# Kernel optimization log

Measured on AMD Instinct MI355X. Metric: run time of the kernel, lower is better.

The kernel has to match this reference:

```python
import jax, jax.numpy as jnp
import numpy as np

N_NODES = 50000
N_EDGES = 800000
NFEAT = 128
NHID = 128
NCLASS = 10
NUM_GRAPHS = 512


def setup_inputs() -> dict:
    key = jax.random.key(0)
    ks = jax.random.split(key, 12)
    x = jax.random.normal(ks[0], (N_NODES, NFEAT), dtype=jnp.float32)
    edge_index = jax.random.randint(ks[1], (2, N_EDGES), 0, N_NODES, dtype=jnp.int64)
    batch = jnp.sort(jax.random.randint(ks[2], (N_NODES,), 0, NUM_GRAPHS, dtype=jnp.int64))
    def glorot(k, fan_in, fan_out):
        lim = np.sqrt(6.0 / (fan_in + fan_out))
        return jax.random.uniform(k, (fan_in, fan_out), jnp.float32, -lim, lim)
    return {
        "x": x, "edge_index": edge_index, "batch": batch,
        "W0": glorot(ks[3], NFEAT, NHID), "b0": jnp.zeros((NHID,), jnp.float32),
        "W1": glorot(ks[4], NHID, NHID), "b1": jnp.zeros((NHID,), jnp.float32),
        "W2": glorot(ks[5], NHID, NHID), "b2": jnp.zeros((NHID,), jnp.float32),
        "lin_w": glorot(ks[6], NHID, NCLASS), "lin_b": jnp.zeros((NCLASS,), jnp.float32),
    }


def _gcn_norm(edge_index, n):
    # PyG GCNConv: add self-loops, symmetric normalization D^-1/2 A D^-1/2
    loop = jnp.arange(n, dtype=edge_index.dtype)
    src = jnp.concatenate([edge_index[0], loop])  # [E+N]
    dst = jnp.concatenate([edge_index[1], loop])
    deg = jax.ops.segment_sum(jnp.ones_like(dst, dtype=jnp.float32), dst, num_segments=n)
    dis = jnp.where(deg > 0, jax.lax.rsqrt(jnp.maximum(deg, 1.0)), 0.0)
    norm = dis[src] * dis[dst]  # [E+N]
    return src, dst, norm


def _gcn_conv(x, W, b, src, dst, norm, n):
    h = x @ W                              # [N, nhid]
    msg = h[src] * norm[:, None]           # gather + scale, [E+N, nhid]
    out = jax.ops.segment_sum(msg, dst, num_segments=n)
    return out + b


def reference(x, edge_index, batch, W0, b0, W1, b1, W2, b2, lin_w, lin_b):
    n = x.shape[0]
    src, dst, norm = _gcn_norm(edge_index, n)
    h = x
    for (W, b) in ((W0, b0), (W1, b1), (W2, b2)):
        h = jax.nn.relu(_gcn_conv(h, W, b, src, dst, norm, n))
    # global mean pool over graphs
    sums = jax.ops.segment_sum(h, batch, num_segments=NUM_GRAPHS)
    cnts = jax.ops.segment_sum(jnp.ones((n,), jnp.float32), batch, num_segments=NUM_GRAPHS)
    pooled = sums / jnp.maximum(cnts, 1.0)[:, None]  # [G, nhid]
    logits = pooled @ lin_w + lin_b
    return jax.nn.log_softmax(logits, axis=-1)
```

## Files before the change

kernel.cpp:

```cpp
#include <hip/hip_runtime.h>
#include <hip/hip_fp16.h>


#define FEAT 128
#define NCLASS 10
#define NB_MAX 512

typedef _Float16 h8 __attribute__((ext_vector_type(8)));
typedef float f4 __attribute__((ext_vector_type(4)));

__device__ inline int swz(int row, int cbyte) { return row * 256 + (cbyte ^ ((row & 7) << 4)); }

__device__ inline void gather_pad8(const h8* __restrict__ Hs, const int* __restrict__ csr,
                                   int s, int e, int lig, float* a0, float* a1) {
  int ep = s + ((e - s + 7) & ~7);
  for (int k = s; k < ep; k += 8) {
    int4 c0 = *(const int4*)&csr[k];
    int4 c1 = *(const int4*)&csr[k + 4];
    h8 v0 = Hs[(size_t)c0.x * 16 + lig];
    h8 v1 = Hs[(size_t)c0.y * 16 + lig];
    h8 v2 = Hs[(size_t)c0.z * 16 + lig];
    h8 v3 = Hs[(size_t)c0.w * 16 + lig];
    h8 v4 = Hs[(size_t)c1.x * 16 + lig];
    h8 v5 = Hs[(size_t)c1.y * 16 + lig];
    h8 v6 = Hs[(size_t)c1.z * 16 + lig];
    h8 v7 = Hs[(size_t)c1.w * 16 + lig];
#pragma unroll
    for (int j = 0; j < 8; ++j) a0[j] += (float)v0[j];
#pragma unroll
    for (int j = 0; j < 8; ++j) a1[j] += (float)v1[j];
#pragma unroll
    for (int j = 0; j < 8; ++j) a0[j] += (float)v2[j];
#pragma unroll
    for (int j = 0; j < 8; ++j) a1[j] += (float)v3[j];
#pragma unroll
    for (int j = 0; j < 8; ++j) a0[j] += (float)v4[j];
#pragma unroll
    for (int j = 0; j < 8; ++j) a1[j] += (float)v5[j];
#pragma unroll
    for (int j = 0; j < 8; ++j) a0[j] += (float)v6[j];
#pragma unroll
    for (int j = 0; j < 8; ++j) a1[j] += (float)v7[j];
  }
}

__global__ void __launch_bounds__(256) prep_kernel(const int* __restrict__ ei,
                                                   int* __restrict__ bhist,
                                                   int ne, int nb, int epb, int hb,
                                                   const float* __restrict__ W0,
                                                   const float* __restrict__ W1,
                                                   const float* __restrict__ W2,
                                                   _Float16* __restrict__ Wt, int wtb,
                                                   const int* __restrict__ batch,
                                                   int* __restrict__ gstart, int n, int g) {
  int t = threadIdx.x;
  if (blockIdx.x >= hb + wtb) {
    int i = (blockIdx.x - hb - wtb) * 256 + t;
    if (i >= n) return;
    int bi = batch[i];
    int bp = (i == 0) ? -1 : batch[i - 1];
    for (int q = bp + 1; q <= bi; ++q) gstart[q] = i;
    if (i == n - 1)
      for (int q = bi + 1; q <= g; ++q) gstart[q] = n;
    return;
  }
  if (blockIdx.x >= hb) {
    int i = (blockIdx.x - hb) * 256 + t;
    if (i < 3 * FEAT * FEAT) {
      int l = i / (FEAT * FEAT);
      int r = i - l * (FEAT * FEAT);
      int nn = r >> 7, kk = r & 127;
      const float* W = (l == 0) ? W0 : (l == 1) ? W1 : W2;
      Wt[i] = (_Float16)W[kk * FEAT + nn];
    }
    return;
  }
  __shared__ int lh[NB_MAX];
  for (int i = t; i < nb; i += 256) lh[i] = 0;
  __syncthreads();
  int r0 = blockIdx.x * epb;
  int r1 = min(r0 + epb, ne);
  for (int k = r0 + t; k < r1; k += 256) atomicAdd(&lh[ei[ne + k] >> 7], 1);
  __syncthreads();
  for (int i = t; i < nb; i += 256)
    if (lh[i]) atomicAdd(&bhist[i], lh[i]);
}

__global__ void __launch_bounds__(512) bscan_kernel(const int* __restrict__ bhist,
                                                    int* __restrict__ bstart,
                                                    int* __restrict__ bcur,
                                                    int nb, int ne) {
  __shared__ int sh[512];
  int t = threadIdx.x;
  int v = (t < nb) ? bhist[t] : 0;
  sh[t] = v;
  __syncthreads();
  int x = v;
  for (int d = 1; d < 512; d <<= 1) {
    int y = (t >= d) ? sh[t - d] : 0;
    __syncthreads();
    x += y;
    sh[t] = x;
    __syncthreads();
  }
  if (t < nb) {
    bstart[t] = x - v;
    bcur[t] = x - v;
  }
  if (t == 0) bstart[nb] = ne;
}

__global__ void __launch_bounds__(256) scatter_kernel(const int* __restrict__ ei,
                                                      int* __restrict__ bcur,
                                                      unsigned* __restrict__ buf,
                                                      int ne, int nb, int epb) {
  __shared__ int lh[NB_MAX], lbs[NB_MAX];
  int t = threadIdx.x;
  for (int i = t; i < nb; i += 256) lh[i] = 0;
  __syncthreads();
  int r0 = blockIdx.x * epb;
  int r1 = min(r0 + epb, ne);
  for (int k = r0 + t; k < r1; k += 256) atomicAdd(&lh[ei[ne + k] >> 7], 1);
  __syncthreads();
  for (int i = t; i < nb; i += 256) {
    int c = lh[i];
    lbs[i] = c ? atomicAdd(&bcur[i], c) : 0;
    lh[i] = 0;
  }
  __syncthreads();
  for (int k = r0 + t; k < r1; k += 256) {
    int src = ei[k];
    int dst = ei[ne + k];
    int b = dst >> 7;
    int p = lbs[b] + atomicAdd(&lh[b], 1);
    buf[p] = (unsigned)src | ((unsigned)(dst & 127) << 25);
  }
}

__global__ void __launch_bounds__(256) bucket_build_kernel(const unsigned* __restrict__ buf,
                                                           const int* __restrict__ bstart,
                                                           int2* __restrict__ offend,
                                                           int* __restrict__ csr,
                                                           float* __restrict__ dis, int n) {
  __shared__ int cnt[128], cur[128], sh[128], ps[128];
  int b = blockIdx.x, t = threadIdx.x;
  int e0 = bstart[b], e1 = bstart[b + 1];
  int pb = ((e0 + 7) & ~7) + 1024 * b;
  if (t < 128) cnt[t] = 0;
  __syncthreads();
  for (int k = e0 + t; k < e1; k += 256) atomicAdd(&cnt[buf[k] >> 25], 1);
  __syncthreads();
  int v = 0, pdv = 0;
  if (t < 128) {
    v = cnt[t];
    pdv = (v + 7) & ~7;
    sh[t] = pdv;
  }
  __syncthreads();
  int x = pdv;
  for (int d = 1; d < 128; d <<= 1) {
    int y = (t < 128 && t >= d) ? sh[t - d] : 0;
    __syncthreads();
    if (t < 128) {
      x += y;
      sh[t] = x;
    }
    __syncthreads();
  }
  if (t < 128) {
    int node = (b << 7) + t;
    int st = x - pdv;
    ps[t] = st;
    cur[t] = st;
    if (node < n) {
      offend[node] = make_int2(pb + st, pb + st + v);
      dis[node] = rsqrtf((float)(v + 1));
    }
  }
  __syncthreads();
  for (int k = e0 + t; k < e1; k += 256) {
    unsigned u = buf[k];
    int d = u >> 25;
    int p = atomicAdd(&cur[d], 1);
    csr[pb + p] = (int)(u & 0x1FFFFFFu);
  }
  __syncthreads();
  if (t < 128) {
    int pd = (cnt[t] + 7) & ~7;
    for (int q = cnt[t]; q < pd; ++q) csr[pb + ps[t] + q] = n;
  }
}

__global__ void __launch_bounds__(256) gemm_mfma_kernel(const float* __restrict__ Xf,
                                                        const _Float16* __restrict__ Wt,
                                                        const float* __restrict__ dis,
                                                        _Float16* __restrict__ Hs, int n) {
  __shared__ _Float16 st[64 * FEAT];
  int tid = threadIdx.x;
  int w = tid >> 6, lane = tid & 63;
  int l15 = lane & 15, hi = lane >> 4;

  int rowA = blockIdx.x * 64 + w * 16 + l15;
  int rA = min(rowA, n - 1);

  f4 acc[8];
#pragma unroll
  for (int nb = 0; nb < 8; ++nb) acc[nb] = (f4)(0.f);

#pragma unroll
  for (int kk = 0; kk < FEAT; kk += 32) {
    int ko = kk + hi * 8;
    h8 a;
    float4 x0 = *(const float4*)&Xf[(size_t)rA * FEAT + ko];
    float4 x1 = *(const float4*)&Xf[(size_t)rA * FEAT + ko + 4];
    a[0] = (_Float16)x0.x; a[1] = (_Float16)x0.y; a[2] = (_Float16)x0.z; a[3] = (_Float16)x0.w;
    a[4] = (_Float16)x1.x; a[5] = (_Float16)x1.y; a[6] = (_Float16)x1.z; a[7] = (_Float16)x1.w;
#pragma unroll
    for (int nb = 0; nb < 8; ++nb) {
      h8 bfr = *(const h8*)&Wt[(nb * 16 + l15) * FEAT + ko];
      acc[nb] = __builtin_amdgcn_mfma_f32_16x16x32_f16(a, bfr, acc[nb], 0, 0, 0);
    }
  }

  float dv[4];
#pragma unroll
  for (int r = 0; r < 4; ++r) {
    int grow = blockIdx.x * 64 + w * 16 + hi * 4 + r;
    dv[r] = dis[min(grow, n - 1)];
  }
#pragma unroll
  for (int nb = 0; nb < 8; ++nb)
#pragma unroll
    for (int r = 0; r < 4; ++r)
      st[(w * 16 + hi * 4 + r) * FEAT + nb * 16 + l15] = (_Float16)(acc[nb][r] * dv[r]);
  __syncthreads();

  int rowbase = blockIdx.x * 64;
#pragma unroll
  for (int i = tid; i < 64 * FEAT / 8; i += 256) {
    int row = rowbase + (i >> 4);
    if (row < n)
      *(uint4*)&Hs[(size_t)row * FEAT + (i & 15) * 8] =
          *(const uint4*)&st[(i >> 4) * FEAT + (i & 15) * 8];
  }
}

__global__ void __launch_bounds__(256) fused_kernel(const h8* __restrict__ Hs_in,
                                                    const int* __restrict__ csr,
                                                    const int2* __restrict__ offend,
                                                    const float* __restrict__ dis,
                                                    const float* __restrict__ bias,
                                                    const _Float16* __restrict__ Wt,
                                                    _Float16* __restrict__ Hs_out, int n) {
  __shared__ char xsb[64 * 256];
  int tid = threadIdx.x;
  int w = tid >> 6, lane = tid & 63;
  int grp = lane >> 4, lig = lane & 15;
  int row0 = blockIdx.x * 64;
  int g16 = w * 4 + grp;

  float4 b0 = ((const float4*)bias)[lig * 2];
  float4 b1 = ((const float4*)bias)[lig * 2 + 1];
  float bb[8] = {b0.x, b0.y, b0.z, b0.w, b1.x, b1.y, b1.z, b1.w};

  for (int m = 0; m < 4; ++m) {
    int ar = g16 * 4 + m;
    int nd = min(row0 + ar, n - 1);
    int2 oe = offend[nd];
    float a0[8], a1[8];
    h8 v = Hs_in[(size_t)nd * 16 + lig];
#pragma unroll
    for (int j = 0; j < 8; ++j) {
      a0[j] = (float)v[j];
      a1[j] = 0.f;
    }
    gather_pad8(Hs_in, csr, oe.x, oe.y, lig, a0, a1);
    float d = dis[nd];
    h8 o;
#pragma unroll
    for (int j = 0; j < 8; ++j)
      o[j] = (_Float16)fmaxf(fmaf(d, a0[j] + a1[j], bb[j]), 0.f);
    *(h8*)(xsb + swz(ar, lig * 16)) = o;
  }
  __syncthreads();

  int l15 = lane & 15, hi = lane >> 4;
  f4 acc[8];
#pragma unroll
  for (int nb = 0; nb < 8; ++nb) acc[nb] = (f4)(0.f);
#pragma unroll
  for (int kk = 0; kk < FEAT; kk += 32) {
    int ko = kk + hi * 8;
    h8 a = *(const h8*)(xsb + swz(w * 16 + l15, ko * 2));
#pragma unroll
    for (int nb = 0; nb < 8; ++nb) {
      h8 bfr = *(const h8*)&Wt[(nb * 16 + l15) * FEAT + ko];
      acc[nb] = __builtin_amdgcn_mfma_f32_16x16x32_f16(a, bfr, acc[nb], 0, 0, 0);
    }
  }

  float dv[4];
#pragma unroll
  for (int r = 0; r < 4; ++r) {
    int grow = row0 + w * 16 + hi * 4 + r;
    dv[r] = dis[min(grow, n - 1)];
  }
  __syncthreads();
#pragma unroll
  for (int nb = 0; nb < 8; ++nb)
#pragma unroll
    for (int r = 0; r < 4; ++r) {
      int srow = w * 16 + hi * 4 + r;
      *(_Float16*)(xsb + swz(srow, (nb * 16 + l15) * 2)) = (_Float16)(acc[nb][r] * dv[r]);
    }
  __syncthreads();
#pragma unroll
  for (int i = tid; i < 64 * FEAT / 8; i += 256) {
    int row = row0 + (i >> 4);
    if (row < n)
      *(uint4*)&Hs_out[(size_t)row * FEAT + (i & 15) * 8] =
          *(const uint4*)(xsb + swz(i >> 4, (i & 15) * 16));
  }
}

__global__ void __launch_bounds__(256) agg_kernel(const h8* __restrict__ Hs,
                                                  const int* __restrict__ csr,
                                                  const int2* __restrict__ offend,
                                                  const float* __restrict__ dis,
                                                  const float* __restrict__ bias,
                                                  h8* __restrict__ out, int n) {
  int tid = threadIdx.x;
  int g16 = tid >> 4, lig = tid & 15;
  int row0 = blockIdx.x * 64;

  float4 b0 = ((const float4*)bias)[lig * 2];
  float4 b1 = ((const float4*)bias)[lig * 2 + 1];
  float bb[8] = {b0.x, b0.y, b0.z, b0.w, b1.x, b1.y, b1.z, b1.w};

  for (int m = 0; m < 4; ++m) {
    int node = row0 + g16 * 4 + m;
    if (node >= n) return;
    int2 oe = offend[node];
    float a0[8], a1[8];
    h8 v = Hs[(size_t)node * 16 + lig];
#pragma unroll
    for (int j = 0; j < 8; ++j) {
      a0[j] = (float)v[j];
      a1[j] = 0.f;
    }
    gather_pad8(Hs, csr, oe.x, oe.y, lig, a0, a1);
    float d = dis[node];
    h8 o;
#pragma unroll
    for (int j = 0; j < 8; ++j)
      o[j] = (_Float16)fmaxf(fmaf(d, a0[j] + a1[j], bb[j]), 0.f);
    out[(size_t)node * 16 + lig] = o;
  }
}

__global__ void __launch_bounds__(128) pool_kernel(const __half* __restrict__ h,
                                                   const int* __restrict__ gstart,
                                                   const float* __restrict__ lw,
                                                   const float* __restrict__ lb,
                                                   float* __restrict__ out) {
  int g = blockIdx.x;
  int t = threadIdx.x;
  int s = gstart[g];
  int e = gstart[g + 1];
  float a0 = 0.f, a1 = 0.f, a2 = 0.f, a3 = 0.f;
  int i = s;
  for (; i + 4 <= e; i += 4) {
    a0 += __half2float(h[(size_t)i * FEAT + t]);
    a1 += __half2float(h[(size_t)(i + 1) * FEAT + t]);
    a2 += __half2float(h[(size_t)(i + 2) * FEAT + t]);
    a3 += __half2float(h[(size_t)(i + 3) * FEAT + t]);
  }
  for (; i < e; ++i) a0 += __half2float(h[(size_t)i * FEAT + t]);
  float acc = a0 + a1 + a2 + a3;
  float cnt = (float)(e - s);
  float pooled = acc / fmaxf(cnt, 1.f);
  __shared__ float lds[FEAT];
  __shared__ float logits[NCLASS];
  lds[t] = pooled;
  __syncthreads();
  if (t < NCLASS) {
    float z = lb[t];
    for (int k = 0; k < FEAT; ++k) z += lds[k] * lw[k * NCLASS + t];
    logits[t] = z;
  }
  __syncthreads();
  if (t < NCLASS) {
    float m = logits[0];
#pragma unroll
    for (int c = 1; c < NCLASS; ++c) m = fmaxf(m, logits[c]);
    float ssum = 0.f;
#pragma unroll
    for (int c = 0; c < NCLASS; ++c) ssum += expf(logits[c] - m);
    out[(size_t)g * NCLASS + t] = logits[t] - m - logf(ssum);
  }
}

extern "C" void kernel_launch(void* const* d_in, const int* in_sizes, int n_in,
                              void* d_out, int out_size, void* d_ws, size_t ws_size,
                              hipStream_t stream) {
  const float* x = (const float*)d_in[0];
  const int* ei = (const int*)d_in[1];
  const int* batch = (const int*)d_in[2];
  const float* W0 = (const float*)d_in[3];
  const float* b0 = (const float*)d_in[4];
  const float* W1 = (const float*)d_in[5];
  const float* b1 = (const float*)d_in[6];
  const float* W2 = (const float*)d_in[7];
  const float* b2 = (const float*)d_in[8];
  const float* lw = (const float*)d_in[9];
  const float* lb = (const float*)d_in[10];

  int n = in_sizes[2];
  int ne = in_sizes[1] / 2;
  int g = out_size / NCLASS;
  int nb = (n + 127) >> 7;
  int hblocks = 120;
  int epb = (ne + hblocks - 1) / hblocks;
  int wtblocks = (3 * FEAT * FEAT + 255) / 256;
  int bndblocks = (n + 255) / 256;

  char* ws = (char*)d_ws;
  size_t p = 0;
  auto alloc = [&](size_t bytes) {
    size_t cur = p;
    p += (bytes + 255) & ~(size_t)255;
    return cur;
  };
  int2* offend = (int2*)(ws + alloc((size_t)n * 8));
  int* csr = (int*)(ws + alloc(((size_t)ne + 1024 * nb + 64) * 4));
  int* bhist = (int*)(ws + alloc((size_t)NB_MAX * 4));
  int* bstart = (int*)(ws + alloc((size_t)(NB_MAX + 1) * 4));
  int* bcur = (int*)(ws + alloc((size_t)NB_MAX * 4));
  int* gstart = (int*)(ws + alloc((size_t)(g + 1) * 4));
  float* dis = (float*)(ws + alloc((size_t)n * 4));
  unsigned* buf = (unsigned*)(ws + alloc((size_t)ne * 4));
  _Float16* Wt = (_Float16*)(ws + alloc((size_t)3 * FEAT * FEAT * 2));
  _Float16* HA = (_Float16*)(ws + alloc((size_t)(n + 1) * FEAT * 2));
  _Float16* HB = (_Float16*)(ws + alloc((size_t)(n + 1) * FEAT * 2));

  hipMemsetAsync(bhist, 0, NB_MAX * 4, stream);
  hipMemsetAsync(HA + (size_t)n * FEAT, 0, FEAT * 2, stream);
  hipMemsetAsync(HB + (size_t)n * FEAT, 0, FEAT * 2, stream);

  prep_kernel<<<hblocks + wtblocks + bndblocks, 256, 0, stream>>>(
      ei, bhist, ne, nb, epb, hblocks, W0, W1, W2, Wt, wtblocks, batch, gstart, n, g);
  bscan_kernel<<<1, 512, 0, stream>>>(bhist, bstart, bcur, nb, ne);
  scatter_kernel<<<hblocks, 256, 0, stream>>>(ei, bcur, buf, ne, nb, epb);
  bucket_build_kernel<<<nb, 256, 0, stream>>>(buf, bstart, offend, csr, dis, n);

  int gblocks = (n + 63) / 64;
  gemm_mfma_kernel<<<gblocks, 256, 0, stream>>>(x, Wt, dis, HA, n);
  fused_kernel<<<gblocks, 256, 0, stream>>>((const h8*)HA, csr, offend, dis, b0,
                                            Wt + (size_t)1 * FEAT * FEAT, HB, n);
  fused_kernel<<<gblocks, 256, 0, stream>>>((const h8*)HB, csr, offend, dis, b1,
                                            Wt + (size_t)2 * FEAT * FEAT, HA, n);
  agg_kernel<<<gblocks, 256, 0, stream>>>((const h8*)HA, csr, offend, dis, b2, (h8*)HB, n);

  pool_kernel<<<g, 128, 0, stream>>>((const __half*)HB, gstart, lw, lb, (float*)d_out);
}
```

Baseline: 225.4 us.

## Double threads per block in GCN aggregation kernels, halving nodes per lane group

The fused and aggregation kernels now launch 512 threads per 64-node block, so each 16-lane group gathers 2 nodes instead of 4. The neighbour gather loop also unrolls by 4 instead of 8. In the fused kernel the 64x128 MFMA tile is split across 8 waves, as 4 row strips times 2 column halves, each holding 4 accumulators. The aim is more waves in flight to hide gather latency and less serial work per thread. The cost is fewer outstanding loads per thread and a tighter register budget from launch_bounds(512,6).

```diff
diff --git a/kernel.cpp b/kernel.cpp
--- a/kernel.cpp
+++ b/kernel.cpp
@@ -11,20 +11,15 @@
 
 __device__ inline int swz(int row, int cbyte) { return row * 256 + (cbyte ^ ((row & 7) << 4)); }
 
-__device__ inline void gather_pad8(const h8* __restrict__ Hs, const int* __restrict__ csr,
+__device__ inline void gather_pad4(const h8* __restrict__ Hs, const int* __restrict__ csr,
                                    int s, int e, int lig, float* a0, float* a1) {
   int ep = s + ((e - s + 7) & ~7);
-  for (int k = s; k < ep; k += 8) {
-    int4 c0 = *(const int4*)&csr[k];
-    int4 c1 = *(const int4*)&csr[k + 4];
-    h8 v0 = Hs[(size_t)c0.x * 16 + lig];
-    h8 v1 = Hs[(size_t)c0.y * 16 + lig];
-    h8 v2 = Hs[(size_t)c0.z * 16 + lig];
-    h8 v3 = Hs[(size_t)c0.w * 16 + lig];
-    h8 v4 = Hs[(size_t)c1.x * 16 + lig];
-    h8 v5 = Hs[(size_t)c1.y * 16 + lig];
-    h8 v6 = Hs[(size_t)c1.z * 16 + lig];
-    h8 v7 = Hs[(size_t)c1.w * 16 + lig];
+  for (int k = s; k < ep; k += 4) {
+    int4 c = *(const int4*)&csr[k];
+    h8 v0 = Hs[(size_t)c.x * 16 + lig];
+    h8 v1 = Hs[(size_t)c.y * 16 + lig];
+    h8 v2 = Hs[(size_t)c.z * 16 + lig];
+    h8 v3 = Hs[(size_t)c.w * 16 + lig];
 #pragma unroll
     for (int j = 0; j < 8; ++j) a0[j] += (float)v0[j];
 #pragma unroll
@@ -33,14 +28,6 @@
     for (int j = 0; j < 8; ++j) a0[j] += (float)v2[j];
 #pragma unroll
     for (int j = 0; j < 8; ++j) a1[j] += (float)v3[j];
-#pragma unroll
-    for (int j = 0; j < 8; ++j) a0[j] += (float)v4[j];
-#pragma unroll
-    for (int j = 0; j < 8; ++j) a1[j] += (float)v5[j];
-#pragma unroll
-    for (int j = 0; j < 8; ++j) a0[j] += (float)v6[j];
-#pragma unroll
-    for (int j = 0; j < 8; ++j) a1[j] += (float)v7[j];
   }
 }
 
@@ -245,26 +232,27 @@
   }
 }
 
-__global__ void __launch_bounds__(256) fused_kernel(const h8* __restrict__ Hs_in,
-                                                    const int* __restrict__ csr,
-                                                    const int2* __restrict__ offend,
-                                                    const float* __restrict__ dis,
-                                                    const float* __restrict__ bias,
-                                                    const _Float16* __restrict__ Wt,
-                                                    _Float16* __restrict__ Hs_out, int n) {
+__global__ void __launch_bounds__(512, 6) fused_kernel(const h8* __restrict__ Hs_in,
+                                                       const int* __restrict__ csr,
+                                                       const int2* __restrict__ offend,
+                                                       const float* __restrict__ dis,
+                                                       const float* __restrict__ bias,
+                                                       const _Float16* __restrict__ Wt,
+                                                       _Float16* __restrict__ Hs_out, int n) {
   __shared__ char xsb[64 * 256];
   int tid = threadIdx.x;
   int w = tid >> 6, lane = tid & 63;
   int grp = lane >> 4, lig = lane & 15;
   int row0 = blockIdx.x * 64;
-  int g16 = w * 4 + grp;
+  int g32 = w * 4 + grp;
 
   float4 b0 = ((const float4*)bias)[lig * 2];
   float4 b1 = ((const float4*)bias)[lig * 2 + 1];
   float bb[8] = {b0.x, b0.y, b0.z, b0.w, b1.x, b1.y, b1.z, b1.w};
 
-  for (int m = 0; m < 4; ++m) {
-    int ar = g16 * 4 + m;
+#pragma unroll
+  for (int m = 0; m < 2; ++m) {
+    int ar = g32 * 2 + m;
     int nd = min(row0 + ar, n - 1);
     int2 oe = offend[nd];
     float a0[8], a1[8];
@@ -274,7 +262,7 @@
       a0[j] = (float)v[j];
       a1[j] = 0.f;
     }
-    gather_pad8(Hs_in, csr, oe.x, oe.y, lig, a0, a1);
+    gather_pad4(Hs_in, csr, oe.x, oe.y, lig, a0, a1);
     float d = dis[nd];
     h8 o;
 #pragma unroll
@@ -285,16 +273,17 @@
   __syncthreads();
 
   int l15 = lane & 15, hi = lane >> 4;
-  f4 acc[8];
-#pragma unroll
-  for (int nb = 0; nb < 8; ++nb) acc[nb] = (f4)(0.f);
+  int strip = w & 3, ch = w >> 2;
+  f4 acc[4];
+#pragma unroll
+  for (int nb = 0; nb < 4; ++nb) acc[nb] = (f4)(0.f);
 #pragma unroll
   for (int kk = 0; kk < FEAT; kk += 32) {
     int ko = kk + hi * 8;
-    h8 a = *(const h8*)(xsb + swz(w * 16 + l15, ko * 2));
-#pragma unroll
-    for (int nb = 0; nb < 8; ++nb) {
-      h8 bfr = *(const h8*)&Wt[(nb * 16 + l15) * FEAT + ko];
+    h8 a = *(const h8*)(xsb + swz(strip * 16 + l15, ko * 2));
+#pragma unroll
+    for (int nb = 0; nb < 4; ++nb) {
+      h8 bfr = *(const h8*)&Wt[(ch * 64 + nb * 16 + l15) * FEAT + ko];
       acc[nb] = __builtin_amdgcn_mfma_f32_16x16x32_f16(a, bfr, acc[nb], 0, 0, 0);
     }
   }
@@ -302,20 +291,21 @@
   float dv[4];
 #pragma unroll
   for (int r = 0; r < 4; ++r) {
-    int grow = row0 + w * 16 + hi * 4 + r;
+    int grow = row0 + strip * 16 + hi * 4 + r;
     dv[r] = dis[min(grow, n - 1)];
   }
   __syncthreads();
 #pragma unroll
-  for (int nb = 0; nb < 8; ++nb)
+  for (int nb = 0; nb < 4; ++nb)
 #pragma unroll
     for (int r = 0; r < 4; ++r) {
-      int srow = w * 16 + hi * 4 + r;
-      *(_Float16*)(xsb + swz(srow, (nb * 16 + l15) * 2)) = (_Float16)(acc[nb][r] * dv[r]);
-    }
-  __syncthreads();
-#pragma unroll
-  for (int i = tid; i < 64 * FEAT / 8; i += 256) {
+      int srow = strip * 16 + hi * 4 + r;
+      *(_Float16*)(xsb + swz(srow, (ch * 64 + nb * 16 + l15) * 2)) =
+          (_Float16)(acc[nb][r] * dv[r]);
+    }
+  __syncthreads();
+#pragma unroll
+  for (int i = tid; i < 64 * FEAT / 8; i += 512) {
     int row = row0 + (i >> 4);
     if (row < n)
       *(uint4*)&Hs_out[(size_t)row * FEAT + (i & 15) * 8] =
@@ -323,38 +313,40 @@
   }
 }
 
-__global__ void __launch_bounds__(256) agg_kernel(const h8* __restrict__ Hs,
-                                                  const int* __restrict__ csr,
-                                                  const int2* __restrict__ offend,
-                                                  const float* __restrict__ dis,
-                                                  const float* __restrict__ bias,
-                                                  h8* __restrict__ out, int n) {
+__global__ void __launch_bounds__(512, 6) agg_kernel(const h8* __restrict__ Hs,
+                                                     const int* __restrict__ csr,
+                                                     const int2* __restrict__ offend,
+                                                     const float* __restrict__ dis,
+                                                     const float* __restrict__ bias,
+                                                     h8* __restrict__ out, int n) {
   int tid = threadIdx.x;
-  int g16 = tid >> 4, lig = tid & 15;
+  int g32 = tid >> 4, lig = tid & 15;
   int row0 = blockIdx.x * 64;
 
   float4 b0 = ((const float4*)bias)[lig * 2];
   float4 b1 = ((const float4*)bias)[lig * 2 + 1];
   float bb[8] = {b0.x, b0.y, b0.z, b0.w, b1.x, b1.y, b1.z, b1.w};
 
-  for (int m = 0; m < 4; ++m) {
-    int node = row0 + g16 * 4 + m;
-    if (node >= n) return;
-    int2 oe = offend[node];
-    float a0[8], a1[8];
-    h8 v = Hs[(size_t)node * 16 + lig];
-#pragma unroll
-    for (int j = 0; j < 8; ++j) {
-      a0[j] = (float)v[j];
-      a1[j] = 0.f;
-    }
-    gather_pad8(Hs, csr, oe.x, oe.y, lig, a0, a1);
-    float d = dis[node];
-    h8 o;
-#pragma unroll
-    for (int j = 0; j < 8; ++j)
-      o[j] = (_Float16)fmaxf(fmaf(d, a0[j] + a1[j], bb[j]), 0.f);
-    out[(size_t)node * 16 + lig] = o;
+#pragma unroll
+  for (int m = 0; m < 2; ++m) {
+    int node = row0 + g32 * 2 + m;
+    if (node < n) {
+      int2 oe = offend[node];
+      float a0[8], a1[8];
+      h8 v = Hs[(size_t)node * 16 + lig];
+#pragma unroll
+      for (int j = 0; j < 8; ++j) {
+        a0[j] = (float)v[j];
+        a1[j] = 0.f;
+      }
+      gather_pad4(Hs, csr, oe.x, oe.y, lig, a0, a1);
+      float d = dis[node];
+      h8 o;
+#pragma unroll
+      for (int j = 0; j < 8; ++j)
+        o[j] = (_Float16)fmaxf(fmaf(d, a0[j] + a1[j], bb[j]), 0.f);
+      out[(size_t)node * 16 + lig] = o;
+    }
   }
 }
 
@@ -455,11 +447,11 @@
 
   int gblocks = (n + 63) / 64;
   gemm_mfma_kernel<<<gblocks, 256, 0, stream>>>(x, Wt, dis, HA, n);
-  fused_kernel<<<gblocks, 256, 0, stream>>>((const h8*)HA, csr, offend, dis, b0,
+  fused_kernel<<<gblocks, 512, 0, stream>>>((const h8*)HA, csr, offend, dis, b0,
                                             Wt + (size_t)1 * FEAT * FEAT, HB, n);
-  fused_kernel<<<gblocks, 256, 0, stream>>>((const h8*)HB, csr, offend, dis, b1,
+  fused_kernel<<<gblocks, 512, 0, stream>>>((const h8*)HB, csr, offend, dis, b1,
                                             Wt + (size_t)2 * FEAT * FEAT, HA, n);
-  agg_kernel<<<gblocks, 256, 0, stream>>>((const h8*)HA, csr, offend, dis, b2, (h8*)HB, n);
+  agg_kernel<<<gblocks, 512, 0, stream>>>((const h8*)HA, csr, offend, dis, b2, (h8*)HB, n);
 
   pool_kernel<<<g, 128, 0, stream>>>((const __half*)HB, gstart, lw, lb, (float*)d_out);
 }
```

Measured after the change: 221.9 us. About the same (-1.6%).
